# Kernel tuning notes

Measured on AMD Instinct MI355X. Metric: run time of the kernel, lower is better.

Reference implementation:

```python
import jax, jax.numpy as jnp
import numpy as np

DIM = 2048
NUM_HEADS = 16
NUM_KV_HEADS = 4
HEAD_DIM = DIM // NUM_HEADS  # 128
ROPE_BASE = 10000.0
CLIP = 31.0
BLOCK = 128


def fake_quant(w):
    """Blockwise int-ish fake quantization, steady QAT state (ratio=1, clip=31, no noise)."""
    out_f, in_f = w.shape
    pad = (-in_f) % BLOCK
    wp = jnp.pad(w, ((0, 0), (0, pad)))
    wb = wp.reshape(-1, BLOCK)
    # scale computed under no_grad in torch -> stop_gradient
    bmax = jnp.max(jnp.abs(wb), axis=1)
    s = jnp.maximum(bmax / CLIP, 1e-12).astype(jnp.float16)
    s = jnp.maximum(s, jnp.finfo(jnp.float16).tiny).astype(jnp.float32)
    s = jax.lax.stop_gradient(s)[:, None]
    ws = wb / s
    q = ws - jax.lax.stop_gradient(ws) + jax.lax.stop_gradient(
        jnp.round(jnp.clip(ws, -(CLIP + 1.0), CLIP)))  # STE
    qw = (q * s).reshape(out_f, in_f + pad)
    return qw[:, :in_f] if pad > 0 else qw


def rms_norm(x):
    eps = jnp.finfo(x.dtype).eps
    return x * jax.lax.rsqrt(jnp.mean(x * x, axis=-1, keepdims=True) + eps)


def rope_tables(seqlen, dtype):
    inv_freq = 1.0 / (ROPE_BASE ** (jnp.arange(0, HEAD_DIM, 2, dtype=jnp.float32) / HEAD_DIM))
    freqs = jnp.outer(jnp.arange(seqlen, dtype=jnp.float32), inv_freq)  # [S, hd/2]
    return jnp.cos(freqs).astype(dtype), jnp.sin(freqs).astype(dtype)


def apply_rotary(x, cos, sin):
    # x: [B,H,S,hd]; cos/sin: [S,hd/2]
    half = x.shape[-1] // 2
    x1, x2 = x[..., :half], x[..., half:]
    return jnp.concatenate((x1 * cos + x2 * sin, -x1 * sin + x2 * cos), axis=-1)


def setup_inputs() -> dict:
    key = jax.random.key(0)
    ks = jax.random.split(key, 6)
    kv_dim = NUM_KV_HEADS * HEAD_DIM
    std = DIM ** -0.5
    return {
        "x": jax.random.normal(ks[0], (2, 2048, DIM), dtype=jnp.float32),
        "Wq": jax.random.normal(ks[1], (DIM, DIM), dtype=jnp.float32) * std,
        "Wk": jax.random.normal(ks[2], (kv_dim, DIM), dtype=jnp.float32) * std,
        "Wv": jax.random.normal(ks[3], (kv_dim, DIM), dtype=jnp.float32) * std,
        "Wproj": jax.random.normal(ks[4], (DIM, DIM), dtype=jnp.float32) * std,
        "q_gain": jnp.full((NUM_HEADS,), 1.0, dtype=jnp.float32),
    }


def reference(x, Wq, Wk, Wv, Wproj, q_gain):
    B, S, D = x.shape
    H, KV, hd = NUM_HEADS, NUM_KV_HEADS, HEAD_DIM
    q = (x @ fake_quant(Wq).T).reshape(B, S, H, hd).transpose(0, 2, 1, 3)   # [B,H,S,hd]
    k = (x @ fake_quant(Wk).T).reshape(B, S, KV, hd).transpose(0, 2, 1, 3)  # [B,KV,S,hd]
    v = (x @ fake_quant(Wv).T).reshape(B, S, KV, hd).transpose(0, 2, 1, 3)
    q = rms_norm(q)
    k = rms_norm(k)
    cos, sin = rope_tables(S, q.dtype)
    q = apply_rotary(q, cos, sin)
    k = apply_rotary(k, cos, sin)
    q = q * q_gain[None, :, None, None]
    # GQA: expand kv heads
    rep = H // KV
    k = jnp.repeat(k, rep, axis=1)  # [B,H,S,hd]
    v = jnp.repeat(v, rep, axis=1)
    scale = 1.0 / jnp.sqrt(jnp.asarray(hd, dtype=q.dtype))
    scores = jnp.einsum("bhqd,bhkd->bhqk", q, k) * scale
    causal = jnp.tril(jnp.ones((S, S), dtype=bool))
    scores = jnp.where(causal, scores, jnp.asarray(-jnp.inf, dtype=scores.dtype))
    attn = jax.nn.softmax(scores, axis=-1)
    y = jnp.einsum("bhqk,bhkd->bhqd", attn, v)  # [B,H,S,hd]
    y = y.transpose(0, 2, 1, 3).reshape(B, S, D)
    return y @ fake_quant(Wproj).T
```

## Files before the change

### kernel.cpp

```cpp
#include <hip/hip_runtime.h>
#include <hip/hip_bf16.h>
#include <hip/hip_fp16.h>

#define SEQ    2048
#define DMODEL 2048
#define NH     16
#define NKV    4
#define HD     128
#define NTOT   3072
#define MROWS  4096

typedef __attribute__((ext_vector_type(4))) float f32x4;
typedef __attribute__((ext_vector_type(8))) __bf16 bf16x8;
typedef __attribute__((ext_vector_type(8))) unsigned short u16x8;
typedef __attribute__((ext_vector_type(4))) unsigned short u16x4;

__device__ __forceinline__ void async_copy16(const void* g, void* l) {
  __builtin_amdgcn_global_load_lds(
      (const __attribute__((address_space(1))) void*)g,
      (__attribute__((address_space(3))) void*)l, 16, 0, 0);
}

__device__ __forceinline__ unsigned short fto16(float f) {
  __hip_bfloat16 h = __float2bfloat16(f);
  return *(unsigned short*)&h;
}

__device__ __forceinline__ float b2f(unsigned short u) {
  unsigned int t = (unsigned int)u << 16;
  float f;
  __builtin_memcpy(&f, &t, 4);
  return f;
}

__global__ __launch_bounds__(256) void fq_kernel(const float* __restrict__ Wq,
                                                 const float* __restrict__ Wk,
                                                 const float* __restrict__ Wv,
                                                 const float* __restrict__ Wp,
                                                 unsigned short* __restrict__ Wcat,
                                                 unsigned short* __restrict__ Wpq) {
  int g = blockIdx.x * 4 + (threadIdx.x >> 6);
  int lane = threadIdx.x & 63;
  const float* W;
  unsigned short* out;
  int blk;
  if (g < 32768)      { W = Wq; out = Wcat;                          blk = g; }
  else if (g < 40960) { W = Wk; out = Wcat + (size_t)2048 * 2048;    blk = g - 32768; }
  else if (g < 49152) { W = Wv; out = Wcat + (size_t)2560 * 2048;    blk = g - 40960; }
  else                { W = Wp; out = Wpq;                           blk = g - 49152; }
  const float* p = W + (size_t)blk * 128 + lane * 2;
  float w0 = p[0], w1 = p[1];
  float m = fmaxf(fabsf(w0), fabsf(w1));
#pragma unroll
  for (int o = 32; o; o >>= 1) m = fmaxf(m, __shfl_xor(m, o));
  float s = fmaxf(m / 31.0f, 1e-12f);
  s = __half2float(__float2half(s));
  s = fmaxf(s, 6.103515625e-05f);
  float q0 = rintf(fminf(fmaxf(w0 / s, -32.0f), 31.0f)) * s;
  float q1 = rintf(fminf(fmaxf(w1 / s, -32.0f), 31.0f)) * s;
  unsigned short* o16 = out + (size_t)blk * 128 + lane * 2;
  o16[0] = fto16(q0);
  o16[1] = fto16(q1);
}

__global__ __launch_bounds__(256) void conv_kernel(const float* __restrict__ in,
                                                   unsigned short* __restrict__ out,
                                                   int n) {
  int i = (blockIdx.x * blockDim.x + threadIdx.x) * 4;
  if (i >= n) return;
  float4 v = *(const float4*)(in + i);
  ushort4 o;
  o.x = fto16(v.x); o.y = fto16(v.y); o.z = fto16(v.z); o.w = fto16(v.w);
  *(ushort4*)(out + i) = o;
}

#define BM 128
#define BN 128
#define BK 64
template <typename OT>
__global__ __launch_bounds__(256, 3) void gemm_bt(const unsigned short* __restrict__ A,
                                                  const unsigned short* __restrict__ Bm,
                                                  OT* __restrict__ C,
                                                  int M, int N, int K) {
  __shared__ unsigned short As[BM * BK];
  __shared__ unsigned short Bs[BN * BK];
  const int tid = threadIdx.x;
  const int wave = tid >> 6, lane = tid & 63;
  const int quad = lane >> 4, l16 = lane & 15;

  int wg = blockIdx.y * gridDim.x + blockIdx.x;
  int nwg = gridDim.x * gridDim.y;
  int cpx = nwg >> 3;
  int swz = (wg & 7) * cpx + (wg >> 3);
  int bxs = swz % gridDim.x, bys = swz / gridDim.x;
  const int m0 = bxs * BM, n0 = bys * BN;
  const int wm = (wave >> 1) * 64, wn = (wave & 1) * 64;

  const unsigned short* Ag = A + (size_t)m0 * K;
  const unsigned short* Bg = Bm + (size_t)n0 * K;

  f32x4 acc[4][4];
#pragma unroll
  for (int i = 0; i < 4; i++)
#pragma unroll
    for (int j = 0; j < 4; j++) acc[i][j] = f32x4{0.f, 0.f, 0.f, 0.f};

  const int srow = tid >> 3;
  const int sg8 = (((lane & 7) ^ (lane >> 3))) * 8;
  const unsigned short* gA = Ag + (size_t)srow * K + sg8;
  const unsigned short* gB = Bg + (size_t)srow * K + sg8;
  unsigned short* lA = &As[wave * 512];
  unsigned short* lB = &Bs[wave * 512];

  for (int k0 = 0; k0 < K; k0 += BK) {
    __syncthreads();
#pragma unroll
    for (int c = 0; c < 4; ++c) async_copy16(gA + (size_t)c * 32 * K + k0, lA + c * 2048);
#pragma unroll
    for (int c = 0; c < 4; ++c) async_copy16(gB + (size_t)c * 32 * K + k0, lB + c * 2048);
    __syncthreads();
#pragma unroll
    for (int kk = 0; kk < 2; ++kk) {
      bf16x8 af[4], bf[4];
#pragma unroll
      for (int t = 0; t < 4; t++)
        af[t] = *(const bf16x8*)&As[(wm + t * 16 + l16) * BK + ((((kk << 2) + quad) ^ (l16 & 7)) << 3)];
#pragma unroll
      for (int t = 0; t < 4; t++)
        bf[t] = *(const bf16x8*)&Bs[(wn + t * 16 + l16) * BK + ((((kk << 2) + quad) ^ (l16 & 7)) << 3)];
#pragma unroll
      for (int i = 0; i < 4; i++)
#pragma unroll
        for (int j = 0; j < 4; j++)
          acc[i][j] = __builtin_amdgcn_mfma_f32_16x16x32_bf16(af[i], bf[j], acc[i][j], 0, 0, 0);
    }
  }
#pragma unroll
  for (int i = 0; i < 4; i++) {
    int row_base = m0 + wm + i * 16 + quad * 4;
#pragma unroll
    for (int j = 0; j < 4; j++) {
      int col = n0 + wn + j * 16 + l16;
#pragma unroll
      for (int r = 0; r < 4; r++) {
        if constexpr (sizeof(OT) == 2)
          C[(size_t)(row_base + r) * N + col] = fto16(acc[i][j][r]);
        else
          C[(size_t)(row_base + r) * N + col] = acc[i][j][r];
      }
    }
  }
}

#define QSCALE 0.12751791437524245f
__global__ __launch_bounds__(256) void normrope_kernel(const unsigned short* __restrict__ qkvb,
                                                       const float* __restrict__ qgain,
                                                       unsigned short* __restrict__ qbuf,
                                                       unsigned short* __restrict__ kbuf) {
  const int i = blockIdx.x;
  const int bz = i >> 11, tok = i & 2047;
  const int wave = threadIdx.x >> 6, lane = threadIdx.x & 63;
  const unsigned short* row = qkvb + (size_t)i * NTOT;

  double invf = pow(10000.0, -(double)(2 * lane) / 128.0);
  float freq = (float)((double)tok * invf);
  float cs = cosf(freq), sn = sinf(freq);

  for (int slot = wave; slot < 20; slot += 4) {
    if (slot < 16) {
      int hh = slot;
      const unsigned short* src = row + hh * HD;
      float x1 = b2f(src[lane]), x2 = b2f(src[lane + 64]);
      float ss = x1 * x1 + x2 * x2;
#pragma unroll
      for (int o = 32; o; o >>= 1) ss += __shfl_xor(ss, o);
      float rn = rsqrtf(ss * (1.0f / 128.0f) + 1.1920929e-07f);
      float n1 = x1 * rn, n2 = x2 * rn;
      float g = qgain[hh] * QSCALE;
      unsigned short* dst = qbuf + ((size_t)(bz * NH + hh) * SEQ + tok) * HD;
      dst[lane]      = fto16((n1 * cs + n2 * sn) * g);
      dst[lane + 64] = fto16((-n1 * sn + n2 * cs) * g);
    } else {
      int hh = slot - 16;
      const unsigned short* src = row + DMODEL + hh * HD;
      float x1 = b2f(src[lane]), x2 = b2f(src[lane + 64]);
      float ss = x1 * x1 + x2 * x2;
#pragma unroll
      for (int o = 32; o; o >>= 1) ss += __shfl_xor(ss, o);
      float rn = rsqrtf(ss * (1.0f / 128.0f) + 1.1920929e-07f);
      float n1 = x1 * rn, n2 = x2 * rn;
      unsigned short* dst = kbuf + ((size_t)(bz * NKV + hh) * SEQ + tok) * HD;
      dst[lane]      = fto16(n1 * cs + n2 * sn);
      dst[lane + 64] = fto16(-n1 * sn + n2 * cs);
    }
  }
}

__global__ __launch_bounds__(256) void vtrans_kernel(const unsigned short* __restrict__ qkvb,
                                                     unsigned short* __restrict__ vtb) {
  __shared__ unsigned short T[64 * 72];
  const int s0 = blockIdx.x * 64;
  const int d0 = blockIdx.y * 64;
  const int bz = blockIdx.z >> 2, h = blockIdx.z & 3;
  const int tid = threadIdx.x;
#pragma unroll
  for (int i = 0; i < 2; ++i) {
    int c = i * 256 + tid;
    int s = c >> 3, ch = c & 7;
    const unsigned short* src =
        qkvb + (size_t)(bz * SEQ + s0 + s) * NTOT + DMODEL + 512 + h * HD + d0 + ch * 8;
    *(u16x8*)&T[s * 72 + ch * 8] = *(const u16x8*)src;
  }
  __syncthreads();
  unsigned short* outg = vtb + (size_t)(bz * NKV + h) * HD * SEQ;
#pragma unroll
  for (int i = 0; i < 2; ++i) {
    int c = i * 256 + tid;
    int d = c >> 3, sc = c & 7;
    u16x8 v;
#pragma unroll
    for (int j = 0; j < 8; ++j) v[j] = T[(sc * 8 + j) * 72 + d];
    *(u16x8*)(outg + (size_t)(d0 + d) * SEQ + s0 + sc * 8) = v;
  }
}

__global__ __launch_bounds__(512, 4) void attn_kernel(const unsigned short* __restrict__ qb,
                                                      const unsigned short* __restrict__ kb,
                                                      const unsigned short* __restrict__ vtb,
                                                      unsigned short* __restrict__ yb) {
  __shared__ unsigned short Ks[2][64 * 128];
  __shared__ unsigned short Vt[128 * 64];
  __shared__ unsigned short Ps[8][16 * 64];

  const int bx = blockIdx.x;
  const int h = blockIdx.y;
  const int bz = blockIdx.z;
  const int qt = bz ? bx : (15 - bx);
  const int tid = threadIdx.x;
  const int wave = tid >> 6, lane = tid & 63;
  const int quad = lane >> 4, l16 = lane & 15;
  const int q0 = qt * 128;
  const int base = q0 + wave * 16;
  const int kdiag = base >> 6;

  const unsigned short* qg = qb + (size_t)(bz * NH + h) * SEQ * HD;
  const unsigned short* kg = kb + (size_t)(bz * NKV + (h >> 2)) * SEQ * HD;
  const unsigned short* vg = vtb + (size_t)(bz * NKV + (h >> 2)) * HD * SEQ;
  unsigned short* psw = &Ps[wave][0];

  bf16x8 qf[4];
#pragma unroll
  for (int ds = 0; ds < 4; ++ds)
    qf[ds] = *(const bf16x8*)(qg + (size_t)(base + l16) * HD + ds * 32 + quad * 8);

  f32x4 oacc[8];
#pragma unroll
  for (int j = 0; j < 8; ++j) oacc[j] = f32x4{0.f, 0.f, 0.f, 0.f};
  float m_i = -__builtin_inff();
  float l_i = 0.f;

  const int krow0 = wave * 4 + (lane >> 4);
  const int ksrcg = (lane & 15) ^ (krow0 & 15);
  const unsigned short* kgK = kg + (size_t)krow0 * HD + ksrcg * 8;

  const int vdw = tid >> 3, vgr = tid & 7;

  const int nkt = 2 * qt + 2;

  async_copy16(kgK, &Ks[0][wave * 512]);
  async_copy16(kgK + (size_t)32 * HD, &Ks[0][4096 + wave * 512]);
  u16x8 pv[2];
#pragma unroll
  for (int i = 0; i < 2; ++i)
    pv[i] = *(const u16x8*)(vg + (size_t)(i * 64 + vdw) * SEQ + vgr * 8);

  for (int kt = 0; kt < nkt; ++kt) {
    __syncthreads();
#pragma unroll
    for (int i = 0; i < 2; ++i) {
      int d = i * 64 + vdw;
      *(u16x8*)&Vt[d * 64 + ((vgr ^ (d & 7)) << 3)] = pv[i];
    }
    if (kt + 1 < nkt) {
      const unsigned short* s = kgK + (size_t)(kt + 1) * 64 * HD;
      async_copy16(s, &Ks[(kt + 1) & 1][wave * 512]);
      async_copy16(s + (size_t)32 * HD, &Ks[(kt + 1) & 1][4096 + wave * 512]);
    }
    __asm__ volatile("s_waitcnt lgkmcnt(0)" ::: "memory");
    __builtin_amdgcn_sched_barrier(0);
    __asm__ volatile("s_barrier" ::: "memory");

    if (kt + 1 < nkt) {
#pragma unroll
      for (int i = 0; i < 2; ++i)
        pv[i] = *(const u16x8*)(vg + (size_t)(i * 64 + vdw) * SEQ + (kt + 1) * 64 + vgr * 8);
    }

    if (kt <= kdiag) {
      const unsigned short* Kc = Ks[kt & 1];
      f32x4 st[4];
#pragma unroll
      for (int mt = 0; mt < 4; ++mt) st[mt] = f32x4{0.f, 0.f, 0.f, 0.f};
      __builtin_amdgcn_s_setprio(1);
#pragma unroll
      for (int mt = 0; mt < 4; ++mt)
#pragma unroll
        for (int ds = 0; ds < 4; ++ds) {
          bf16x8 kf = *(const bf16x8*)&Kc[(mt * 16 + l16) * 128 + ((((ds << 2) + quad) ^ l16) << 3)];
          st[mt] = __builtin_amdgcn_mfma_f32_16x16x32_bf16(kf, qf[ds], st[mt], 0, 0, 0);
        }
      __builtin_amdgcn_s_setprio(0);

      const int qrow = base + l16;
      float p[4][4];
      float mx = -__builtin_inff();
      if (kt == kdiag) {
#pragma unroll
        for (int mt = 0; mt < 4; ++mt)
#pragma unroll
          for (int r = 0; r < 4; ++r) {
            int kp = kt * 64 + mt * 16 + quad * 4 + r;
            float v = (kp <= qrow) ? st[mt][r] : -__builtin_inff();
            p[mt][r] = v;
            mx = fmaxf(mx, v);
          }
      } else {
#pragma unroll
        for (int mt = 0; mt < 4; ++mt)
#pragma unroll
          for (int r = 0; r < 4; ++r) {
            p[mt][r] = st[mt][r];
            mx = fmaxf(mx, st[mt][r]);
          }
      }
      mx = fmaxf(mx, __shfl_xor(mx, 16));
      mx = fmaxf(mx, __shfl_xor(mx, 32));
      float mnew = (mx > m_i + 8.f) ? mx : m_i;
      float rs = 0.f;
#pragma unroll
      for (int mt = 0; mt < 4; ++mt)
#pragma unroll
        for (int r = 0; r < 4; ++r) {
          float e = exp2f(p[mt][r] - mnew);
          p[mt][r] = e;
          rs += e;
        }
      rs += __shfl_xor(rs, 16);
      rs += __shfl_xor(rs, 32);
      if (mnew != m_i) {
        float a = exp2f(m_i - mnew);
#pragma unroll
        for (int j = 0; j < 8; ++j) oacc[j] *= a;
        l_i = l_i * a + rs;
        m_i = mnew;
      } else {
        l_i += rs;
      }

#pragma unroll
      for (int mt = 0; mt < 4; ++mt) {
        u16x4 w;
#pragma unroll
        for (int r = 0; r < 4; ++r) w[r] = fto16(p[mt][r]);
        int g = mt * 2 + (quad >> 1);
        *(u16x4*)&psw[l16 * 64 + ((g ^ (l16 & 7)) << 3) + (quad & 1) * 4] = w;
      }

      __asm__ volatile("s_waitcnt lgkmcnt(0)" ::: "memory");

      __builtin_amdgcn_s_setprio(1);
#pragma unroll
      for (int c = 0; c < 2; ++c) {
        bf16x8 pf = *(const bf16x8*)&psw[l16 * 64 + ((((c << 2) + quad) ^ (l16 & 7)) << 3)];
#pragma unroll
        for (int mt = 0; mt < 8; ++mt) {
          bf16x8 vf = *(const bf16x8*)&Vt[(mt * 16 + l16) * 64 + ((((c << 2) + quad) ^ (l16 & 7)) << 3)];
          oacc[mt] = __builtin_amdgcn_mfma_f32_16x16x32_bf16(vf, pf, oacc[mt], 0, 0, 0);
        }
      }
      __builtin_amdgcn_s_setprio(0);
    }
  }

  {
    float il = 1.0f / l_i;
    int qrow = base + l16;
#pragma unroll
    for (int mt = 0; mt < 8; ++mt) {
      u16x4 o;
#pragma unroll
      for (int r = 0; r < 4; ++r) o[r] = fto16(oacc[mt][r] * il);
      *(u16x4*)&yb[(size_t)(bz * SEQ + qrow) * DMODEL + h * HD + mt * 16 + quad * 4] = o;
    }
  }
}

extern "C" void kernel_launch(void* const* d_in, const int* in_sizes, int n_in,
                              void* d_out, int out_size, void* d_ws, size_t ws_size,
                              hipStream_t stream) {
  (void)in_sizes; (void)n_in; (void)out_size; (void)ws_size;
  const float* x  = (const float*)d_in[0];
  const float* Wq = (const float*)d_in[1];
  const float* Wk = (const float*)d_in[2];
  const float* Wv = (const float*)d_in[3];
  const float* Wp = (const float*)d_in[4];
  const float* qg = (const float*)d_in[5];
  float* out = (float*)d_out;
  char* ws = (char*)d_ws;

  unsigned short* xb   = (unsigned short*)(ws + 0);
  unsigned short* Wcat = (unsigned short*)(ws + 16777216);
  unsigned short* Wpq  = (unsigned short*)(ws + 29360128);
  unsigned short* qkvb = (unsigned short*)(ws + 37748736);
  unsigned short* qbuf = (unsigned short*)(ws + 62914560);
  unsigned short* kbuf = (unsigned short*)(ws + 79691776);
  unsigned short* vtb  = (unsigned short*)(ws + 83886080);
  unsigned short* yb   = xb;

  fq_kernel<<<81920 / 4, 256, 0, stream>>>(Wq, Wk, Wv, Wp, Wcat, Wpq);
  conv_kernel<<<8388608 / 1024, 256, 0, stream>>>(x, xb, 8388608);
  gemm_bt<unsigned short><<<dim3(32, 24), 256, 0, stream>>>(xb, Wcat, qkvb, MROWS, NTOT, DMODEL);
  normrope_kernel<<<MROWS, 256, 0, stream>>>(qkvb, qg, qbuf, kbuf);
  vtrans_kernel<<<dim3(32, 2, 8), 256, 0, stream>>>(qkvb, vtb);
  attn_kernel<<<dim3(16, NH, 2), 512, 0, stream>>>(qbuf, kbuf, vtb, yb);
  gemm_bt<float><<<dim3(32, 16), 256, 0, stream>>>(yb, Wpq, out, MROWS, DMODEL, DMODEL);
}
```

Before: 309.4 us.

## Rewrite attention with 32x32 MFMA, register-resident P, async double-buffered V

The attention kernel moves from 16x16x32 to 32x32x16 bf16 MFMA, with each of 4 waves handling 32 query rows (256 threads instead of 512). The softmax probabilities stay in registers: they are packed with v_cvt_pk_bf16_f32 and rearranged with v_permlane32_swap instead of a round trip through LDS. V tiles are now loaded with async global-to-LDS copies into a double buffer, like K, which removes the register staging and the explicit lgkmcnt waits. This should cut LDS traffic and instruction count, but it raises register pressure and halves the threads per block, which may lower occupancy.

```diff
diff --git a/kernel.cpp b/kernel.cpp
--- a/kernel.cpp
+++ b/kernel.cpp
@@ -11,6 +11,7 @@
 #define MROWS  4096
 
 typedef __attribute__((ext_vector_type(4))) float f32x4;
+typedef __attribute__((ext_vector_type(16))) float f32x16;
 typedef __attribute__((ext_vector_type(8))) __bf16 bf16x8;
 typedef __attribute__((ext_vector_type(8))) unsigned short u16x8;
 typedef __attribute__((ext_vector_type(4))) unsigned short u16x4;
@@ -31,6 +32,12 @@
   float f;
   __builtin_memcpy(&f, &t, 4);
   return f;
+}
+
+__device__ __forceinline__ unsigned int cvtpk(float lo, float hi) {
+  unsigned int d;
+  asm("v_cvt_pk_bf16_f32 %0, %1, %2" : "=v"(d) : "v"(lo), "v"(hi));
+  return d;
 }
 
 __global__ __launch_bounds__(256) void fq_kernel(const float* __restrict__ Wq,
@@ -224,13 +231,12 @@
   }
 }
 
-__global__ __launch_bounds__(512, 4) void attn_kernel(const unsigned short* __restrict__ qb,
+__global__ __launch_bounds__(256, 2) void attn_kernel(const unsigned short* __restrict__ qb,
                                                       const unsigned short* __restrict__ kb,
                                                       const unsigned short* __restrict__ vtb,
                                                       unsigned short* __restrict__ yb) {
   __shared__ unsigned short Ks[2][64 * 128];
-  __shared__ unsigned short Vt[128 * 64];
-  __shared__ unsigned short Ps[8][16 * 64];
+  __shared__ unsigned short Vt[2][128 * 64];
 
   const int bx = blockIdx.x;
   const int h = blockIdx.y;
@@ -238,160 +244,168 @@
   const int qt = bz ? bx : (15 - bx);
   const int tid = threadIdx.x;
   const int wave = tid >> 6, lane = tid & 63;
-  const int quad = lane >> 4, l16 = lane & 15;
-  const int q0 = qt * 128;
-  const int base = q0 + wave * 16;
+  const int l31 = lane & 31, hi = lane >> 5;
+  const int base = qt * 128 + wave * 32;
   const int kdiag = base >> 6;
+  const int qrow = base + l31;
 
   const unsigned short* qg = qb + (size_t)(bz * NH + h) * SEQ * HD;
   const unsigned short* kg = kb + (size_t)(bz * NKV + (h >> 2)) * SEQ * HD;
   const unsigned short* vg = vtb + (size_t)(bz * NKV + (h >> 2)) * HD * SEQ;
-  unsigned short* psw = &Ps[wave][0];
-
-  bf16x8 qf[4];
-#pragma unroll
-  for (int ds = 0; ds < 4; ++ds)
-    qf[ds] = *(const bf16x8*)(qg + (size_t)(base + l16) * HD + ds * 32 + quad * 8);
-
-  f32x4 oacc[8];
-#pragma unroll
-  for (int j = 0; j < 8; ++j) oacc[j] = f32x4{0.f, 0.f, 0.f, 0.f};
+
+  bf16x8 qf[8];
+#pragma unroll
+  for (int s = 0; s < 8; ++s)
+    qf[s] = *(const bf16x8*)(qg + (size_t)qrow * HD + s * 16 + hi * 8);
+
+  f32x16 oacc[4];
+#pragma unroll
+  for (int i = 0; i < 4; ++i)
+#pragma unroll
+    for (int j = 0; j < 16; ++j) oacc[i][j] = 0.f;
   float m_i = -__builtin_inff();
   float l_i = 0.f;
 
-  const int krow0 = wave * 4 + (lane >> 4);
-  const int ksrcg = (lane & 15) ^ (krow0 & 15);
-  const unsigned short* kgK = kg + (size_t)krow0 * HD + ksrcg * 8;
-
-  const int vdw = tid >> 3, vgr = tid & 7;
+  const int ksub = lane >> 4;
+  const int vsub = lane >> 3;
+  const int vsg = (lane & 7) ^ vsub;
 
   const int nkt = 2 * qt + 2;
 
-  async_copy16(kgK, &Ks[0][wave * 512]);
-  async_copy16(kgK + (size_t)32 * HD, &Ks[0][4096 + wave * 512]);
-  u16x8 pv[2];
-#pragma unroll
-  for (int i = 0; i < 2; ++i)
-    pv[i] = *(const u16x8*)(vg + (size_t)(i * 64 + vdw) * SEQ + vgr * 8);
+#pragma unroll
+  for (int i = 0; i < 4; ++i) {
+    int r = wave * 16 + i * 4 + ksub;
+    async_copy16(kg + (size_t)r * HD + (((lane & 15) ^ (i * 4 + ksub)) << 3),
+                 &Ks[0][(wave * 4 + i) * 512]);
+  }
+#pragma unroll
+  for (int i = 0; i < 4; ++i) {
+    int d = wave * 32 + i * 8 + vsub;
+    async_copy16(vg + (size_t)d * SEQ + (vsg << 3), &Vt[0][(wave * 4 + i) * 512]);
+  }
 
   for (int kt = 0; kt < nkt; ++kt) {
     __syncthreads();
-#pragma unroll
-    for (int i = 0; i < 2; ++i) {
-      int d = i * 64 + vdw;
-      *(u16x8*)&Vt[d * 64 + ((vgr ^ (d & 7)) << 3)] = pv[i];
-    }
     if (kt + 1 < nkt) {
-      const unsigned short* s = kgK + (size_t)(kt + 1) * 64 * HD;
-      async_copy16(s, &Ks[(kt + 1) & 1][wave * 512]);
-      async_copy16(s + (size_t)32 * HD, &Ks[(kt + 1) & 1][4096 + wave * 512]);
-    }
-    __asm__ volatile("s_waitcnt lgkmcnt(0)" ::: "memory");
-    __builtin_amdgcn_sched_barrier(0);
-    __asm__ volatile("s_barrier" ::: "memory");
-
-    if (kt + 1 < nkt) {
-#pragma unroll
-      for (int i = 0; i < 2; ++i)
-        pv[i] = *(const u16x8*)(vg + (size_t)(i * 64 + vdw) * SEQ + (kt + 1) * 64 + vgr * 8);
-    }
-
-    if (kt <= kdiag) {
-      const unsigned short* Kc = Ks[kt & 1];
-      f32x4 st[4];
-#pragma unroll
-      for (int mt = 0; mt < 4; ++mt) st[mt] = f32x4{0.f, 0.f, 0.f, 0.f};
-      __builtin_amdgcn_s_setprio(1);
-#pragma unroll
-      for (int mt = 0; mt < 4; ++mt)
-#pragma unroll
-        for (int ds = 0; ds < 4; ++ds) {
-          bf16x8 kf = *(const bf16x8*)&Kc[(mt * 16 + l16) * 128 + ((((ds << 2) + quad) ^ l16) << 3)];
-          st[mt] = __builtin_amdgcn_mfma_f32_16x16x32_bf16(kf, qf[ds], st[mt], 0, 0, 0);
+      int b = (kt + 1) & 1;
+#pragma unroll
+      for (int i = 0; i < 4; ++i) {
+        int r = wave * 16 + i * 4 + ksub;
+        async_copy16(kg + (size_t)((kt + 1) * 64 + r) * HD + (((lane & 15) ^ (i * 4 + ksub)) << 3),
+                     &Ks[b][(wave * 4 + i) * 512]);
+      }
+#pragma unroll
+      for (int i = 0; i < 4; ++i) {
+        int d = wave * 32 + i * 8 + vsub;
+        async_copy16(vg + (size_t)d * SEQ + (kt + 1) * 64 + (vsg << 3),
+                     &Vt[b][(wave * 4 + i) * 512]);
+      }
+    }
+    if (kt > kdiag) continue;
+
+    const unsigned short* Kc = Ks[kt & 1];
+    const unsigned short* Vc = Vt[kt & 1];
+
+    f32x16 st[2];
+#pragma unroll
+    for (int mt = 0; mt < 2; ++mt)
+#pragma unroll
+      for (int j = 0; j < 16; ++j) st[mt][j] = 0.f;
+    __builtin_amdgcn_s_setprio(1);
+#pragma unroll
+    for (int mt = 0; mt < 2; ++mt)
+#pragma unroll
+      for (int ds = 0; ds < 8; ++ds) {
+        bf16x8 kf = *(const bf16x8*)&Kc[(mt * 32 + l31) * 128 + ((((ds << 1) + hi) ^ (lane & 15)) << 3)];
+        st[mt] = __builtin_amdgcn_mfma_f32_32x32x16_bf16(kf, qf[ds], st[mt], 0, 0, 0);
+      }
+    __builtin_amdgcn_s_setprio(0);
+
+    float mx = -__builtin_inff();
+    if (kt == kdiag) {
+#pragma unroll
+      for (int mt = 0; mt < 2; ++mt)
+#pragma unroll
+        for (int r = 0; r < 16; ++r) {
+          int kp = kt * 64 + mt * 32 + (r & 3) + 8 * (r >> 2) + 4 * hi;
+          float v = (kp <= qrow) ? st[mt][r] : -__builtin_inff();
+          st[mt][r] = v;
+          mx = fmaxf(mx, v);
         }
-      __builtin_amdgcn_s_setprio(0);
-
-      const int qrow = base + l16;
-      float p[4][4];
-      float mx = -__builtin_inff();
-      if (kt == kdiag) {
-#pragma unroll
-        for (int mt = 0; mt < 4; ++mt)
-#pragma unroll
-          for (int r = 0; r < 4; ++r) {
-            int kp = kt * 64 + mt * 16 + quad * 4 + r;
-            float v = (kp <= qrow) ? st[mt][r] : -__builtin_inff();
-            p[mt][r] = v;
-            mx = fmaxf(mx, v);
-          }
-      } else {
-#pragma unroll
-        for (int mt = 0; mt < 4; ++mt)
-#pragma unroll
-          for (int r = 0; r < 4; ++r) {
-            p[mt][r] = st[mt][r];
-            mx = fmaxf(mx, st[mt][r]);
-          }
-      }
-      mx = fmaxf(mx, __shfl_xor(mx, 16));
-      mx = fmaxf(mx, __shfl_xor(mx, 32));
-      float mnew = (mx > m_i + 8.f) ? mx : m_i;
-      float rs = 0.f;
-#pragma unroll
-      for (int mt = 0; mt < 4; ++mt)
-#pragma unroll
-        for (int r = 0; r < 4; ++r) {
-          float e = exp2f(p[mt][r] - mnew);
-          p[mt][r] = e;
-          rs += e;
-        }
-      rs += __shfl_xor(rs, 16);
-      rs += __shfl_xor(rs, 32);
-      if (mnew != m_i) {
-        float a = exp2f(m_i - mnew);
-#pragma unroll
-        for (int j = 0; j < 8; ++j) oacc[j] *= a;
-        l_i = l_i * a + rs;
-        m_i = mnew;
-      } else {
-        l_i += rs;
-      }
-
-#pragma unroll
-      for (int mt = 0; mt < 4; ++mt) {
-        u16x4 w;
-#pragma unroll
-        for (int r = 0; r < 4; ++r) w[r] = fto16(p[mt][r]);
-        int g = mt * 2 + (quad >> 1);
-        *(u16x4*)&psw[l16 * 64 + ((g ^ (l16 & 7)) << 3) + (quad & 1) * 4] = w;
-      }
-
-      __asm__ volatile("s_waitcnt lgkmcnt(0)" ::: "memory");
-
-      __builtin_amdgcn_s_setprio(1);
-#pragma unroll
-      for (int c = 0; c < 2; ++c) {
-        bf16x8 pf = *(const bf16x8*)&psw[l16 * 64 + ((((c << 2) + quad) ^ (l16 & 7)) << 3)];
-#pragma unroll
-        for (int mt = 0; mt < 8; ++mt) {
-          bf16x8 vf = *(const bf16x8*)&Vt[(mt * 16 + l16) * 64 + ((((c << 2) + quad) ^ (l16 & 7)) << 3)];
-          oacc[mt] = __builtin_amdgcn_mfma_f32_16x16x32_bf16(vf, pf, oacc[mt], 0, 0, 0);
-        }
-      }
-      __builtin_amdgcn_s_setprio(0);
-    }
+    } else {
+#pragma unroll
+      for (int mt = 0; mt < 2; ++mt)
+#pragma unroll
+        for (int r = 0; r < 16; ++r) mx = fmaxf(mx, st[mt][r]);
+    }
+    mx = fmaxf(mx, __shfl_xor(mx, 32));
+    float mnew = (mx > m_i + 8.f) ? mx : m_i;
+    float rs = 0.f;
+#pragma unroll
+    for (int mt = 0; mt < 2; ++mt)
+#pragma unroll
+      for (int r = 0; r < 16; ++r) {
+        float e = exp2f(st[mt][r] - mnew);
+        st[mt][r] = e;
+        rs += e;
+      }
+    rs += __shfl_xor(rs, 32);
+    if (mnew != m_i) {
+      float a = exp2f(m_i - mnew);
+#pragma unroll
+      for (int i = 0; i < 4; ++i)
+#pragma unroll
+        for (int j = 0; j < 16; ++j) oacc[i][j] *= a;
+      l_i = l_i * a + rs;
+      m_i = mnew;
+    } else {
+      l_i += rs;
+    }
+
+    unsigned int pd[4][4];
+#pragma unroll
+    for (int mt = 0; mt < 2; ++mt)
+#pragma unroll
+      for (int half = 0; half < 2; ++half) {
+        const int rb = half * 8;
+        unsigned int a0 = cvtpk(st[mt][rb + 0], st[mt][rb + 1]);
+        unsigned int b0 = cvtpk(st[mt][rb + 4], st[mt][rb + 5]);
+        unsigned int a1 = cvtpk(st[mt][rb + 2], st[mt][rb + 3]);
+        unsigned int b1 = cvtpk(st[mt][rb + 6], st[mt][rb + 7]);
+        asm("v_permlane32_swap_b32 %0, %1" : "+v"(a0), "+v"(b0));
+        asm("v_permlane32_swap_b32 %0, %1" : "+v"(a1), "+v"(b1));
+        pd[mt * 2 + half][0] = a0;
+        pd[mt * 2 + half][1] = a1;
+        pd[mt * 2 + half][2] = b0;
+        pd[mt * 2 + half][3] = b1;
+      }
+
+    __builtin_amdgcn_s_setprio(1);
+#pragma unroll
+    for (int s = 0; s < 4; ++s) {
+      union { unsigned int u[4]; bf16x8 v; } pb;
+#pragma unroll
+      for (int j = 0; j < 4; ++j) pb.u[j] = pd[s][j];
+#pragma unroll
+      for (int mt2 = 0; mt2 < 4; ++mt2) {
+        bf16x8 vf = *(const bf16x8*)&Vc[(mt2 * 32 + l31) * 64 + ((((s << 1) + hi) ^ (lane & 7)) << 3)];
+        oacc[mt2] = __builtin_amdgcn_mfma_f32_32x32x16_bf16(vf, pb.v, oacc[mt2], 0, 0, 0);
+      }
+    }
+    __builtin_amdgcn_s_setprio(0);
   }
 
   {
     float il = 1.0f / l_i;
-    int qrow = base + l16;
-#pragma unroll
-    for (int mt = 0; mt < 8; ++mt) {
-      u16x4 o;
-#pragma unroll
-      for (int r = 0; r < 4; ++r) o[r] = fto16(oacc[mt][r] * il);
-      *(u16x4*)&yb[(size_t)(bz * SEQ + qrow) * DMODEL + h * HD + mt * 16 + quad * 4] = o;
-    }
+#pragma unroll
+    for (int mt2 = 0; mt2 < 4; ++mt2)
+#pragma unroll
+      for (int u = 0; u < 4; ++u) {
+        u16x4 o;
+#pragma unroll
+        for (int r = 0; r < 4; ++r) o[r] = fto16(oacc[mt2][u * 4 + r] * il);
+        *(u16x4*)&yb[(size_t)(bz * SEQ + qrow) * DMODEL + h * HD + mt2 * 32 + u * 8 + hi * 4] = o;
+      }
   }
 }
 
@@ -422,6 +436,6 @@
   gemm_bt<unsigned short><<<dim3(32, 24), 256, 0, stream>>>(xb, Wcat, qkvb, MROWS, NTOT, DMODEL);
   normrope_kernel<<<MROWS, 256, 0, stream>>>(qkvb, qg, qbuf, kbuf);
   vtrans_kernel<<<dim3(32, 2, 8), 256, 0, stream>>>(qkvb, vtb);
-  attn_kernel<<<dim3(16, NH, 2), 512, 0, stream>>>(qbuf, kbuf, vtb, yb);
+  attn_kernel<<<dim3(16, NH, 2), 256, 0, stream>>>(qbuf, kbuf, vtb, yb);
   gemm_bt<float><<<dim3(32, 16), 256, 0, stream>>>(yb, Wpq, out, MROWS, DMODEL, DMODEL);
 }
```

Result: no change. 314.5 us (+1.6%).

## Pair short and long 64-row query tiles per block for causal load balance

Applied to the files above, without the earlier changes.

Each attention block now has 4 waves and handles two 64-row query tiles, tile px and tile 31-px, one after the other. Every block therefore does the same total number of key tiles, which evens out the causal triangular work. Before, the 128-row tiles with 8 waves skipped work per wave past the diagonal. The first tile's last iteration prefetches tile 0 of K and V for the second pass. In exchange there are fewer waves per block, the Q fragments for both tiles are held in registers, and the key/value stream is loaded twice per block.

```diff
diff --git a/kernel.cpp b/kernel.cpp
--- a/kernel.cpp
+++ b/kernel.cpp
@@ -224,175 +224,201 @@
   }
 }
 
-__global__ __launch_bounds__(512, 4) void attn_kernel(const unsigned short* __restrict__ qb,
+__global__ __launch_bounds__(256, 2) void attn_kernel(const unsigned short* __restrict__ qb,
                                                       const unsigned short* __restrict__ kb,
                                                       const unsigned short* __restrict__ vtb,
                                                       unsigned short* __restrict__ yb) {
   __shared__ unsigned short Ks[2][64 * 128];
   __shared__ unsigned short Vt[128 * 64];
-  __shared__ unsigned short Ps[8][16 * 64];
-
-  const int bx = blockIdx.x;
+  __shared__ unsigned short Ps[4][16 * 64];
+
+  const int px = blockIdx.x;
   const int h = blockIdx.y;
   const int bz = blockIdx.z;
-  const int qt = bz ? bx : (15 - bx);
   const int tid = threadIdx.x;
   const int wave = tid >> 6, lane = tid & 63;
   const int quad = lane >> 4, l16 = lane & 15;
-  const int q0 = qt * 128;
-  const int base = q0 + wave * 16;
-  const int kdiag = base >> 6;
+
+  const int qtA = px, qtB = 31 - px;
+  const int nktA = qtA + 1, nktB = qtB + 1;
+  const int baseA = qtA * 64 + wave * 16;
+  const int baseB = qtB * 64 + wave * 16;
 
   const unsigned short* qg = qb + (size_t)(bz * NH + h) * SEQ * HD;
   const unsigned short* kg = kb + (size_t)(bz * NKV + (h >> 2)) * SEQ * HD;
   const unsigned short* vg = vtb + (size_t)(bz * NKV + (h >> 2)) * HD * SEQ;
   unsigned short* psw = &Ps[wave][0];
 
-  bf16x8 qf[4];
-#pragma unroll
-  for (int ds = 0; ds < 4; ++ds)
-    qf[ds] = *(const bf16x8*)(qg + (size_t)(base + l16) * HD + ds * 32 + quad * 8);
+  bf16x8 qfA[4], qfB[4];
+#pragma unroll
+  for (int ds = 0; ds < 4; ++ds) {
+    qfA[ds] = *(const bf16x8*)(qg + (size_t)(baseA + l16) * HD + ds * 32 + quad * 8);
+    qfB[ds] = *(const bf16x8*)(qg + (size_t)(baseB + l16) * HD + ds * 32 + quad * 8);
+  }
 
   f32x4 oacc[8];
+  float m_i, l_i;
+
+  const int krow_lo = wave * 4 + (lane >> 4);
+  const int ksrcg = (lane & 15) ^ krow_lo;
+  const unsigned short* kgK = kg + (size_t)krow_lo * HD + ksrcg * 8;
+
+  const int vdw = tid >> 3, vgr = tid & 7;
+  const int vslot = (vgr ^ (vdw & 7)) << 3;
+  u16x8 pv[4];
+
+#define STAGE_K(t, b)                                                           \
+  {                                                                             \
+    _Pragma("unroll") for (int i_ = 0; i_ < 4; ++i_)                            \
+        async_copy16(kgK + (size_t)((t) * 64 + i_ * 16) * HD,                   \
+                     &Ks[(b)][i_ * 2048 + wave * 512]);                         \
+  }
+#define LOAD_V(t)                                                               \
+  {                                                                             \
+    _Pragma("unroll") for (int i_ = 0; i_ < 4; ++i_)                            \
+        pv[i_] = *(const u16x8*)(vg + (size_t)(i_ * 32 + vdw) * SEQ + (t) * 64 + vgr * 8); \
+  }
+#define WRITE_V()                                                               \
+  {                                                                             \
+    _Pragma("unroll") for (int i_ = 0; i_ < 4; ++i_)                            \
+        *(u16x8*)&Vt[(i_ * 32 + vdw) * 64 + vslot] = pv[i_];                    \
+  }
+
+  auto do_tile = [&](int kt, int qt, int buf, const bf16x8 (&qf)[4], int base) {
+    const unsigned short* Kc = Ks[buf];
+    f32x4 st[4];
+#pragma unroll
+    for (int mt = 0; mt < 4; ++mt) st[mt] = f32x4{0.f, 0.f, 0.f, 0.f};
+    __builtin_amdgcn_s_setprio(1);
+#pragma unroll
+    for (int mt = 0; mt < 4; ++mt)
+#pragma unroll
+      for (int ds = 0; ds < 4; ++ds) {
+        bf16x8 kf = *(const bf16x8*)&Kc[(mt * 16 + l16) * 128 + ((((ds << 2) + quad) ^ l16) << 3)];
+        st[mt] = __builtin_amdgcn_mfma_f32_16x16x32_bf16(kf, qf[ds], st[mt], 0, 0, 0);
+      }
+    __builtin_amdgcn_s_setprio(0);
+
+    const int qrow = base + l16;
+    float p[4][4];
+    float mx = -__builtin_inff();
+    if (kt == qt) {
+#pragma unroll
+      for (int mt = 0; mt < 4; ++mt)
+#pragma unroll
+        for (int r = 0; r < 4; ++r) {
+          int kp = kt * 64 + mt * 16 + quad * 4 + r;
+          float v = (kp <= qrow) ? st[mt][r] : -__builtin_inff();
+          p[mt][r] = v;
+          mx = fmaxf(mx, v);
+        }
+    } else {
+#pragma unroll
+      for (int mt = 0; mt < 4; ++mt)
+#pragma unroll
+        for (int r = 0; r < 4; ++r) {
+          p[mt][r] = st[mt][r];
+          mx = fmaxf(mx, st[mt][r]);
+        }
+    }
+    mx = fmaxf(mx, __shfl_xor(mx, 16));
+    mx = fmaxf(mx, __shfl_xor(mx, 32));
+    float mnew = (mx > m_i + 8.f) ? mx : m_i;
+    float rs = 0.f;
+#pragma unroll
+    for (int mt = 0; mt < 4; ++mt)
+#pragma unroll
+      for (int r = 0; r < 4; ++r) {
+        float e = exp2f(p[mt][r] - mnew);
+        p[mt][r] = e;
+        rs += e;
+      }
+    rs += __shfl_xor(rs, 16);
+    rs += __shfl_xor(rs, 32);
+    if (mnew != m_i) {
+      float a = exp2f(m_i - mnew);
+#pragma unroll
+      for (int j = 0; j < 8; ++j) oacc[j] *= a;
+      l_i = l_i * a + rs;
+      m_i = mnew;
+    } else {
+      l_i += rs;
+    }
+
+#pragma unroll
+    for (int mt = 0; mt < 4; ++mt) {
+      u16x4 w;
+#pragma unroll
+      for (int r = 0; r < 4; ++r) w[r] = fto16(p[mt][r]);
+      int g2 = mt * 2 + (quad >> 1);
+      *(u16x4*)&psw[l16 * 64 + ((g2 ^ (l16 & 7)) << 3) + (quad & 1) * 4] = w;
+    }
+    __asm__ volatile("s_waitcnt lgkmcnt(0)" ::: "memory");
+
+    __builtin_amdgcn_s_setprio(1);
+#pragma unroll
+    for (int c = 0; c < 2; ++c) {
+      bf16x8 pf = *(const bf16x8*)&psw[l16 * 64 + ((((c << 2) + quad) ^ (l16 & 7)) << 3)];
+#pragma unroll
+      for (int mt = 0; mt < 8; ++mt) {
+        bf16x8 vf = *(const bf16x8*)&Vt[(mt * 16 + l16) * 64 + ((((c << 2) + quad) ^ (l16 & 7)) << 3)];
+        oacc[mt] = __builtin_amdgcn_mfma_f32_16x16x32_bf16(vf, pf, oacc[mt], 0, 0, 0);
+      }
+    }
+    __builtin_amdgcn_s_setprio(0);
+  };
+
+  auto epilogue = [&](int base) {
+    float il = 1.0f / l_i;
+    int qrow = base + l16;
+#pragma unroll
+    for (int mt = 0; mt < 8; ++mt) {
+      u16x4 o;
+#pragma unroll
+      for (int r = 0; r < 4; ++r) o[r] = fto16(oacc[mt][r] * il);
+      *(u16x4*)&yb[(size_t)(bz * SEQ + qrow) * DMODEL + h * HD + mt * 16 + quad * 4] = o;
+    }
+  };
+
+  STAGE_K(0, 0);
+  LOAD_V(0);
+
+  int g = 0;
+  m_i = -__builtin_inff(); l_i = 0.f;
 #pragma unroll
   for (int j = 0; j < 8; ++j) oacc[j] = f32x4{0.f, 0.f, 0.f, 0.f};
-  float m_i = -__builtin_inff();
-  float l_i = 0.f;
-
-  const int krow0 = wave * 4 + (lane >> 4);
-  const int ksrcg = (lane & 15) ^ (krow0 & 15);
-  const unsigned short* kgK = kg + (size_t)krow0 * HD + ksrcg * 8;
-
-  const int vdw = tid >> 3, vgr = tid & 7;
-
-  const int nkt = 2 * qt + 2;
-
-  async_copy16(kgK, &Ks[0][wave * 512]);
-  async_copy16(kgK + (size_t)32 * HD, &Ks[0][4096 + wave * 512]);
-  u16x8 pv[2];
-#pragma unroll
-  for (int i = 0; i < 2; ++i)
-    pv[i] = *(const u16x8*)(vg + (size_t)(i * 64 + vdw) * SEQ + vgr * 8);
-
-  for (int kt = 0; kt < nkt; ++kt) {
+#pragma unroll 1
+  for (int kt = 0; kt < nktA; ++kt, ++g) {
     __syncthreads();
-#pragma unroll
-    for (int i = 0; i < 2; ++i) {
-      int d = i * 64 + vdw;
-      *(u16x8*)&Vt[d * 64 + ((vgr ^ (d & 7)) << 3)] = pv[i];
-    }
-    if (kt + 1 < nkt) {
-      const unsigned short* s = kgK + (size_t)(kt + 1) * 64 * HD;
-      async_copy16(s, &Ks[(kt + 1) & 1][wave * 512]);
-      async_copy16(s + (size_t)32 * HD, &Ks[(kt + 1) & 1][4096 + wave * 512]);
-    }
+    WRITE_V();
+    int nt = (kt + 1 < nktA) ? kt + 1 : 0;
+    STAGE_K(nt, (g + 1) & 1);
     __asm__ volatile("s_waitcnt lgkmcnt(0)" ::: "memory");
     __builtin_amdgcn_sched_barrier(0);
     __asm__ volatile("s_barrier" ::: "memory");
-
-    if (kt + 1 < nkt) {
-#pragma unroll
-      for (int i = 0; i < 2; ++i)
-        pv[i] = *(const u16x8*)(vg + (size_t)(i * 64 + vdw) * SEQ + (kt + 1) * 64 + vgr * 8);
-    }
-
-    if (kt <= kdiag) {
-      const unsigned short* Kc = Ks[kt & 1];
-      f32x4 st[4];
-#pragma unroll
-      for (int mt = 0; mt < 4; ++mt) st[mt] = f32x4{0.f, 0.f, 0.f, 0.f};
-      __builtin_amdgcn_s_setprio(1);
-#pragma unroll
-      for (int mt = 0; mt < 4; ++mt)
-#pragma unroll
-        for (int ds = 0; ds < 4; ++ds) {
-          bf16x8 kf = *(const bf16x8*)&Kc[(mt * 16 + l16) * 128 + ((((ds << 2) + quad) ^ l16) << 3)];
-          st[mt] = __builtin_amdgcn_mfma_f32_16x16x32_bf16(kf, qf[ds], st[mt], 0, 0, 0);
-        }
-      __builtin_amdgcn_s_setprio(0);
-
-      const int qrow = base + l16;
-      float p[4][4];
-      float mx = -__builtin_inff();
-      if (kt == kdiag) {
-#pragma unroll
-        for (int mt = 0; mt < 4; ++mt)
-#pragma unroll
-          for (int r = 0; r < 4; ++r) {
-            int kp = kt * 64 + mt * 16 + quad * 4 + r;
-            float v = (kp <= qrow) ? st[mt][r] : -__builtin_inff();
-            p[mt][r] = v;
-            mx = fmaxf(mx, v);
-          }
-      } else {
-#pragma unroll
-        for (int mt = 0; mt < 4; ++mt)
-#pragma unroll
-          for (int r = 0; r < 4; ++r) {
-            p[mt][r] = st[mt][r];
-            mx = fmaxf(mx, st[mt][r]);
-          }
-      }
-      mx = fmaxf(mx, __shfl_xor(mx, 16));
-      mx = fmaxf(mx, __shfl_xor(mx, 32));
-      float mnew = (mx > m_i + 8.f) ? mx : m_i;
-      float rs = 0.f;
-#pragma unroll
-      for (int mt = 0; mt < 4; ++mt)
-#pragma unroll
-        for (int r = 0; r < 4; ++r) {
-          float e = exp2f(p[mt][r] - mnew);
-          p[mt][r] = e;
-          rs += e;
-        }
-      rs += __shfl_xor(rs, 16);
-      rs += __shfl_xor(rs, 32);
-      if (mnew != m_i) {
-        float a = exp2f(m_i - mnew);
-#pragma unroll
-        for (int j = 0; j < 8; ++j) oacc[j] *= a;
-        l_i = l_i * a + rs;
-        m_i = mnew;
-      } else {
-        l_i += rs;
-      }
-
-#pragma unroll
-      for (int mt = 0; mt < 4; ++mt) {
-        u16x4 w;
-#pragma unroll
-        for (int r = 0; r < 4; ++r) w[r] = fto16(p[mt][r]);
-        int g = mt * 2 + (quad >> 1);
-        *(u16x4*)&psw[l16 * 64 + ((g ^ (l16 & 7)) << 3) + (quad & 1) * 4] = w;
-      }
-
-      __asm__ volatile("s_waitcnt lgkmcnt(0)" ::: "memory");
-
-      __builtin_amdgcn_s_setprio(1);
-#pragma unroll
-      for (int c = 0; c < 2; ++c) {
-        bf16x8 pf = *(const bf16x8*)&psw[l16 * 64 + ((((c << 2) + quad) ^ (l16 & 7)) << 3)];
-#pragma unroll
-        for (int mt = 0; mt < 8; ++mt) {
-          bf16x8 vf = *(const bf16x8*)&Vt[(mt * 16 + l16) * 64 + ((((c << 2) + quad) ^ (l16 & 7)) << 3)];
-          oacc[mt] = __builtin_amdgcn_mfma_f32_16x16x32_bf16(vf, pf, oacc[mt], 0, 0, 0);
-        }
-      }
-      __builtin_amdgcn_s_setprio(0);
-    }
-  }
-
-  {
-    float il = 1.0f / l_i;
-    int qrow = base + l16;
-#pragma unroll
-    for (int mt = 0; mt < 8; ++mt) {
-      u16x4 o;
-#pragma unroll
-      for (int r = 0; r < 4; ++r) o[r] = fto16(oacc[mt][r] * il);
-      *(u16x4*)&yb[(size_t)(bz * SEQ + qrow) * DMODEL + h * HD + mt * 16 + quad * 4] = o;
-    }
-  }
+    LOAD_V(nt);
+    do_tile(kt, qtA, g & 1, qfA, baseA);
+  }
+  epilogue(baseA);
+
+  m_i = -__builtin_inff(); l_i = 0.f;
+#pragma unroll
+  for (int j = 0; j < 8; ++j) oacc[j] = f32x4{0.f, 0.f, 0.f, 0.f};
+#pragma unroll 1
+  for (int kt = 0; kt < nktB; ++kt, ++g) {
+    __syncthreads();
+    WRITE_V();
+    if (kt + 1 < nktB) STAGE_K(kt + 1, (g + 1) & 1);
+    __asm__ volatile("s_waitcnt lgkmcnt(0)" ::: "memory");
+    __builtin_amdgcn_sched_barrier(0);
+    __asm__ volatile("s_barrier" ::: "memory");
+    if (kt + 1 < nktB) LOAD_V(kt + 1);
+    do_tile(kt, qtB, g & 1, qfB, baseB);
+  }
+  epilogue(baseB);
+#undef STAGE_K
+#undef LOAD_V
+#undef WRITE_V
 }
 
 extern "C" void kernel_launch(void* const* d_in, const int* in_sizes, int n_in,
@@ -422,6 +448,6 @@
   gemm_bt<unsigned short><<<dim3(32, 24), 256, 0, stream>>>(xb, Wcat, qkvb, MROWS, NTOT, DMODEL);
   normrope_kernel<<<MROWS, 256, 0, stream>>>(qkvb, qg, qbuf, kbuf);
   vtrans_kernel<<<dim3(32, 2, 8), 256, 0, stream>>>(qkvb, vtb);
-  attn_kernel<<<dim3(16, NH, 2), 512, 0, stream>>>(qbuf, kbuf, vtb, yb);
+  attn_kernel<<<dim3(16, NH, 2), 256, 0, stream>>>(qbuf, kbuf, vtb, yb);
   gemm_bt<float><<<dim3(32, 16), 256, 0, stream>>>(yb, Wpq, out, MROWS, DMODEL, DMODEL);
 }
```

Result: no change. 313.2 us (+1.2%).

## Use 256x256 double-buffered GEMM tiles with async LDS prefetch and MFMA priority

Applied to the files above, without the earlier changes.

Replaces the 128x128 single-buffered GEMM with a 512-thread 256x256 tile kernel that double-buffers LDS. The next K-tile is prefetched asynchronously while MFMAs run on the current one. Raw s_barrier/vmcnt waits and s_setprio wrap the MFMA bursts, and B fragments are reused across A sub-tiles. The aim is to raise arithmetic intensity and overlap loads with compute. The cost is far fewer workgroups (192 and 128), which may leave many CUs idle on this GPU.

```diff
diff --git a/kernel.cpp b/kernel.cpp
--- a/kernel.cpp
+++ b/kernel.cpp
@@ -74,16 +74,15 @@
   *(ushort4*)(out + i) = o;
 }
 
-#define BM 128
-#define BN 128
+#define BM 256
+#define BN 256
 #define BK 64
 template <typename OT>
-__global__ __launch_bounds__(256, 3) void gemm_bt(const unsigned short* __restrict__ A,
+__global__ __launch_bounds__(512, 1) void gemm_bt(const unsigned short* __restrict__ A,
                                                   const unsigned short* __restrict__ Bm,
                                                   OT* __restrict__ C,
                                                   int M, int N, int K) {
-  __shared__ unsigned short As[BM * BK];
-  __shared__ unsigned short Bs[BN * BK];
+  __shared__ unsigned short S[2][2][16384];
   const int tid = threadIdx.x;
   const int wave = tid >> 6, lane = tid & 63;
   const int quad = lane >> 4, l16 = lane & 15;
@@ -94,49 +93,79 @@
   int swz = (wg & 7) * cpx + (wg >> 3);
   int bxs = swz % gridDim.x, bys = swz / gridDim.x;
   const int m0 = bxs * BM, n0 = bys * BN;
-  const int wm = (wave >> 1) * 64, wn = (wave & 1) * 64;
+  const int wm = (wave >> 2) * 128;
+  const int wn = (wave & 3) * 64;
 
   const unsigned short* Ag = A + (size_t)m0 * K;
   const unsigned short* Bg = Bm + (size_t)n0 * K;
 
-  f32x4 acc[4][4];
-#pragma unroll
-  for (int i = 0; i < 4; i++)
+  f32x4 acc[8][4];
+#pragma unroll
+  for (int i = 0; i < 8; i++)
 #pragma unroll
     for (int j = 0; j < 4; j++) acc[i][j] = f32x4{0.f, 0.f, 0.f, 0.f};
 
-  const int srow = tid >> 3;
-  const int sg8 = (((lane & 7) ^ (lane >> 3))) * 8;
+  const int srow = wave * 8 + (lane >> 3);
+  const int sg8 = ((lane & 7) ^ (lane >> 3)) * 8;
   const unsigned short* gA = Ag + (size_t)srow * K + sg8;
   const unsigned short* gB = Bg + (size_t)srow * K + sg8;
-  unsigned short* lA = &As[wave * 512];
-  unsigned short* lB = &Bs[wave * 512];
-
-  for (int k0 = 0; k0 < K; k0 += BK) {
-    __syncthreads();
-#pragma unroll
-    for (int c = 0; c < 4; ++c) async_copy16(gA + (size_t)c * 32 * K + k0, lA + c * 2048);
-#pragma unroll
-    for (int c = 0; c < 4; ++c) async_copy16(gB + (size_t)c * 32 * K + k0, lB + c * 2048);
-    __syncthreads();
-#pragma unroll
-    for (int kk = 0; kk < 2; ++kk) {
-      bf16x8 af[4], bf[4];
-#pragma unroll
-      for (int t = 0; t < 4; t++)
-        af[t] = *(const bf16x8*)&As[(wm + t * 16 + l16) * BK + ((((kk << 2) + quad) ^ (l16 & 7)) << 3)];
-#pragma unroll
-      for (int t = 0; t < 4; t++)
-        bf[t] = *(const bf16x8*)&Bs[(wn + t * 16 + l16) * BK + ((((kk << 2) + quad) ^ (l16 & 7)) << 3)];
-#pragma unroll
-      for (int i = 0; i < 4; i++)
-#pragma unroll
-        for (int j = 0; j < 4; j++)
-          acc[i][j] = __builtin_amdgcn_mfma_f32_16x16x32_bf16(af[i], bf[j], acc[i][j], 0, 0, 0);
-    }
-  }
-#pragma unroll
-  for (int i = 0; i < 4; i++) {
+  const int ldsw = wave * 512;
+
+#define STAGE(t, b)                                                             \
+  {                                                                             \
+    _Pragma("unroll") for (int c_ = 0; c_ < 4; ++c_)                            \
+        async_copy16(gA + (size_t)c_ * 64 * K + (t) * BK, &S[(b)][0][c_ * 4096 + ldsw]); \
+    _Pragma("unroll") for (int c_ = 0; c_ < 4; ++c_)                            \
+        async_copy16(gB + (size_t)c_ * 64 * K + (t) * BK, &S[(b)][1][c_ * 4096 + ldsw]); \
+  }
+
+  const int nt = K >> 6;
+  STAGE(0, 0);
+
+#pragma unroll 1
+  for (int t = 0; t < nt; ++t) {
+    __asm__ volatile("s_barrier" ::: "memory");
+    if (t + 1 < nt) {
+      STAGE(t + 1, (t + 1) & 1);
+      __asm__ volatile("s_waitcnt vmcnt(8)" ::: "memory");
+    } else {
+      __asm__ volatile("s_waitcnt vmcnt(0)" ::: "memory");
+    }
+    __builtin_amdgcn_sched_barrier(0);
+
+    const unsigned short* As = &S[t & 1][0][0];
+    const unsigned short* Bs = &S[t & 1][1][0];
+
+    bf16x8 bf[4][2];
+#pragma unroll
+    for (int j = 0; j < 4; ++j)
+#pragma unroll
+      for (int kk = 0; kk < 2; ++kk)
+        bf[j][kk] = *(const bf16x8*)&Bs[(wn + j * 16 + l16) * 64 + ((((kk << 2) + quad) ^ (l16 & 7)) << 3)];
+
+#pragma unroll
+    for (int q = 0; q < 4; ++q) {
+      bf16x8 af[2][2];
+#pragma unroll
+      for (int i2 = 0; i2 < 2; ++i2)
+#pragma unroll
+        for (int kk = 0; kk < 2; ++kk)
+          af[i2][kk] = *(const bf16x8*)&As[(wm + (q * 2 + i2) * 16 + l16) * 64 + ((((kk << 2) + quad) ^ (l16 & 7)) << 3)];
+      __builtin_amdgcn_s_setprio(1);
+#pragma unroll
+      for (int i2 = 0; i2 < 2; ++i2)
+#pragma unroll
+        for (int j = 0; j < 4; ++j)
+#pragma unroll
+          for (int kk = 0; kk < 2; ++kk)
+            acc[q * 2 + i2][j] = __builtin_amdgcn_mfma_f32_16x16x32_bf16(af[i2][kk], bf[j][kk], acc[q * 2 + i2][j], 0, 0, 0);
+      __builtin_amdgcn_s_setprio(0);
+    }
+  }
+#undef STAGE
+
+#pragma unroll
+  for (int i = 0; i < 8; i++) {
     int row_base = m0 + wm + i * 16 + quad * 4;
 #pragma unroll
     for (int j = 0; j < 4; j++) {
@@ -419,9 +448,9 @@
 
   fq_kernel<<<81920 / 4, 256, 0, stream>>>(Wq, Wk, Wv, Wp, Wcat, Wpq);
   conv_kernel<<<8388608 / 1024, 256, 0, stream>>>(x, xb, 8388608);
-  gemm_bt<unsigned short><<<dim3(32, 24), 256, 0, stream>>>(xb, Wcat, qkvb, MROWS, NTOT, DMODEL);
+  gemm_bt<unsigned short><<<dim3(16, 12), 512, 0, stream>>>(xb, Wcat, qkvb, MROWS, NTOT, DMODEL);
   normrope_kernel<<<MROWS, 256, 0, stream>>>(qkvb, qg, qbuf, kbuf);
   vtrans_kernel<<<dim3(32, 2, 8), 256, 0, stream>>>(qkvb, vtb);
   attn_kernel<<<dim3(16, NH, 2), 512, 0, stream>>>(qbuf, kbuf, vtb, yb);
-  gemm_bt<float><<<dim3(32, 16), 256, 0, stream>>>(yb, Wpq, out, MROWS, DMODEL, DMODEL);
-}
+  gemm_bt<float><<<dim3(16, 8), 512, 0, stream>>>(yb, Wpq, out, MROWS, DMODEL, DMODEL);
+}
```

Result: slower. 318.0 us (+2.8%).
